# Performance work log

Hardware: AMD Instinct MI355X
Metric: run time of the kernel (lower is better)

The kernel has to match this reference:

```python
import jax, jax.numpy as jnp
import numpy as np

D = 1024
B, N = 4, 2048

def setup_inputs() -> dict:
    key = jax.random.key(0)
    ks = jax.random.split(key, 7)
    sc = 1.0 / np.sqrt(D)
    return {
        "x": jax.random.normal(ks[0], (B, N, D), dtype=jnp.float32),
        "wq_w": jax.random.normal(ks[1], (D, D), dtype=jnp.float32) * sc,
        "wq_b": jax.random.normal(ks[2], (D,), dtype=jnp.float32) * 0.01,
        "wk_w": jax.random.normal(ks[3], (D, D), dtype=jnp.float32) * sc,
        "wk_b": jax.random.normal(ks[4], (D,), dtype=jnp.float32) * 0.01,
        "wv_w": jax.random.normal(ks[5], (D, D), dtype=jnp.float32) * sc,
        "wv_b": jax.random.normal(ks[6], (D,), dtype=jnp.float32) * 0.01,
    }

def reference(x, wq_w, wq_b, wk_w, wk_b, wv_w, wv_b):
    # torch Linear: y = x @ W^T + b
    q = x @ wq_w.T + wq_b
    k = x @ wk_w.T + wk_b
    v = x @ wv_w.T + wv_b
    d = q.shape[-1]
    s = jnp.einsum("bid,bjd->bij", q, k) / jnp.sqrt(jnp.float32(d))
    # faithful to original: triu then transpose (zeros, NOT -inf, enter the softmax)
    t = jnp.swapaxes(jnp.triu(s), -2, -1)
    p = jax.nn.softmax(t, axis=-2)
    attn = jnp.swapaxes(jnp.triu(p), -2, -1) @ v
    return attn
```

## Files before the change

kernel.cpp:

```cpp
#include <hip/hip_runtime.h>
#include <hip/hip_fp16.h>
#include <cstdint>

typedef _Float16 half8_t __attribute__((ext_vector_type(8)));
typedef float f32x4 __attribute__((ext_vector_type(4)));

#define D_ 1024
#define B_ 4
#define N_ 2048
#define M_ (B_*N_)
#define NC_ 3072

#define OFF_WCAT  0u
#define OFF_BCAT  6291456u
#define OFF_XB    6303744u
#define OFF_Q     23080960u
#define OFF_K     39858176u
#define OFF_V     56635392u
#define OFF_ZP    73412608u
#define OFF_DEXP  74461184u
#define OFF_SV    74493952u

__device__ __forceinline__ void gload_lds16(const void* g, void* l) {
  __builtin_amdgcn_global_load_lds(
      (const __attribute__((address_space(1))) unsigned int*)(uintptr_t)g,
      (__attribute__((address_space(3))) unsigned int*)(uintptr_t)l, 16, 0, 0);
}

__device__ __forceinline__ void stage128x64(const __half* rowbase, char* lds, int tid) {
#pragma unroll
  for (int inst = 0; inst < 4; ++inst) {
    int L  = inst * 4096 + tid * 16;
    int r  = L >> 7;
    int cb = L & 127;
    int cbs = cb ^ ((r & 7) << 4);
    gload_lds16((const char*)rowbase + (size_t)r * (D_ * 2) + cbs, lds + L);
  }
}

__device__ __forceinline__ half8_t ldsfrag(const char* lds, int row, int cbyte) {
  int b = (row << 7) + (cbyte ^ ((row & 7) << 4));
  return *reinterpret_cast<const half8_t*>(lds + b);
}

__device__ __forceinline__ void gemm128_core(const __half* Arow0, const __half* Brow0,
                                             char* As, char* Bs, f32x4 acc[4][4]) {
  const int tid  = threadIdx.x;
  const int lane = tid & 63;
  const int wave = tid >> 6;
  const int wm = wave >> 1, wn = wave & 1;
  for (int kt = 0; kt < 16; ++kt) {
    if (kt) __syncthreads();
    stage128x64(Arow0 + kt * 64, As, tid);
    stage128x64(Brow0 + kt * 64, Bs, tid);
    asm volatile("s_waitcnt vmcnt(0)" ::: "memory");
    __syncthreads();
#pragma unroll
    for (int kk = 0; kk < 2; ++kk) {
      const int cbyte = kk * 64 + (lane >> 4) * 16;
      half8_t a[4], b[4];
#pragma unroll
      for (int mf = 0; mf < 4; ++mf) a[mf] = ldsfrag(As, wm * 64 + mf * 16 + (lane & 15), cbyte);
#pragma unroll
      for (int nf = 0; nf < 4; ++nf) b[nf] = ldsfrag(Bs, wn * 64 + nf * 16 + (lane & 15), cbyte);
#pragma unroll
      for (int mf = 0; mf < 4; ++mf)
#pragma unroll
        for (int nf = 0; nf < 4; ++nf)
          acc[mf][nf] = __builtin_amdgcn_mfma_f32_16x16x32_f16(a[mf], b[nf], acc[mf][nf], 0, 0, 0);
    }
  }
}

__device__ __forceinline__ void calc_soff(int tid, int soff[4]) {
#pragma unroll
  for (int i = 0; i < 4; ++i) {
    int L = i * 8192 + tid * 16;
    int s = L >> 10;
    int w = L & 1023;
    w ^= ((w >> 9) & 1) << 5;
    int r  = (s >> 1) * 16 + (w >> 6);
    int kb = (s & 1) * 64 + (w & 63);
    soff[i] = r * 2048 + kb;
  }
}

#define MFMA_QUAD(QM, QN)                                                     \
  _Pragma("unroll")                                                           \
  for (int ks = 0; ks < 2; ++ks)                                              \
    _Pragma("unroll")                                                         \
    for (int mf = 0; mf < 4; ++mf)                                            \
      _Pragma("unroll")                                                       \
      for (int nf = 0; nf < 2; ++nf)                                          \
        acc[(QM)*4 + mf][(QN)*2 + nf] = __builtin_amdgcn_mfma_f32_16x16x32_f16( \
            a[mf][ks], b[(QN)][nf][ks], acc[(QM)*4 + mf][(QN)*2 + nf], 0, 0, 0);

__device__ __forceinline__ void gemm256_8ph(const char* Ag, const char* Bg,
                                            char* smem, f32x4 acc[8][4]) {
  const int tid  = threadIdx.x;
  const int lane = tid & 63;
  const int wave = tid >> 6;
  const int wm = wave >> 2, wn = wave & 3;

  int soff[4];
  calc_soff(tid, soff);
  const int wlane = (((lane & 15) * 64 + (lane >> 4) * 16)) ^ (((lane >> 3) & 1) << 5);

#pragma unroll
  for (int i = 0; i < 4; ++i) gload_lds16(Ag + soff[i], smem + i * 8192 + tid * 16);
#pragma unroll
  for (int i = 0; i < 4; ++i) gload_lds16(Bg + soff[i], smem + 32768 + i * 8192 + tid * 16);
  asm volatile("s_waitcnt vmcnt(0)" ::: "memory");
  __builtin_amdgcn_s_barrier();

  for (int t = 0; t < 16; ++t) {
    char* A0  = smem + ((t & 1) << 16);
    char* B0  = A0 + 32768;
    char* A1  = smem + (((t + 1) & 1) << 16);
    char* B1s = A1 + 32768;
    const half8_t* ap = (const half8_t*)(A0 + wm * 16384 + wlane);
    const half8_t* bp = (const half8_t*)(B0 + wn * 8192 + wlane);
    const char* Agn = Ag + (t + 1) * 128;
    const char* Bgn = Bg + (t + 1) * 128;
    const bool pre = (t < 15);

    half8_t a[4][2];
    half8_t b[2][2][2];

#pragma unroll
    for (int mf = 0; mf < 4; ++mf)
#pragma unroll
      for (int ks = 0; ks < 2; ++ks)
        a[mf][ks] = ap[(mf * 2 + ks) * 64];
#pragma unroll
    for (int nf = 0; nf < 2; ++nf)
#pragma unroll
      for (int ks = 0; ks < 2; ++ks)
        b[0][nf][ks] = bp[(nf * 2 + ks) * 64];
    if (pre) {
#pragma unroll
      for (int i = 0; i < 4; ++i) gload_lds16(Agn + soff[i], A1 + i * 8192 + tid * 16);
    }
    __builtin_amdgcn_s_barrier();
    asm volatile("s_waitcnt lgkmcnt(0)" ::: "memory");
    __builtin_amdgcn_s_setprio(1);
    MFMA_QUAD(0, 0)
    __builtin_amdgcn_s_setprio(0);
    __builtin_amdgcn_s_barrier();

#pragma unroll
    for (int nf = 0; nf < 2; ++nf)
#pragma unroll
      for (int ks = 0; ks < 2; ++ks)
        b[1][nf][ks] = bp[((2 + nf) * 2 + ks) * 64];
    if (pre) {
#pragma unroll
      for (int i = 0; i < 4; ++i) gload_lds16(Bgn + soff[i], B1s + i * 8192 + tid * 16);
    }
    __builtin_amdgcn_s_barrier();
    asm volatile("s_waitcnt lgkmcnt(0)" ::: "memory");
    __builtin_amdgcn_s_setprio(1);
    MFMA_QUAD(0, 1)
    __builtin_amdgcn_s_setprio(0);
    __builtin_amdgcn_s_barrier();

#pragma unroll
    for (int mf = 0; mf < 4; ++mf)
#pragma unroll
      for (int ks = 0; ks < 2; ++ks)
        a[mf][ks] = ap[((4 + mf) * 2 + ks) * 64];
    __builtin_amdgcn_s_barrier();
    asm volatile("s_waitcnt lgkmcnt(0)" ::: "memory");
    __builtin_amdgcn_s_setprio(1);
    MFMA_QUAD(1, 0)
    __builtin_amdgcn_s_setprio(0);
    __builtin_amdgcn_s_barrier();

    __builtin_amdgcn_s_setprio(1);
    MFMA_QUAD(1, 1)
    __builtin_amdgcn_s_setprio(0);
    if (pre) asm volatile("s_waitcnt vmcnt(0)" ::: "memory");
    __builtin_amdgcn_s_barrier();
  }
}

__global__ __launch_bounds__(256) void k_prep(
    const float* __restrict__ x, const float* __restrict__ wq, const float* __restrict__ wk,
    const float* __restrict__ wv, const float* __restrict__ bq, const float* __restrict__ bk,
    const float* __restrict__ bv, __half* __restrict__ xb, __half* __restrict__ wcat,
    float* __restrict__ bcat) {
  const int NX4 = (M_ * D_) / 4;
  const int NW4 = (D_ * D_) / 4;
  const int TOT = NX4 + 3 * NW4;
  int tid0 = blockIdx.x * 256 + threadIdx.x;
  int stride = gridDim.x * 256;
  for (int i = tid0; i < TOT; i += stride) {
    float4 f; __half* dst;
    if (i < NX4) {
      f = ((const float4*)x)[i];
      dst = xb + 4 * (size_t)i;
    } else {
      int j = i - NX4; int w = j / NW4; int o = j - w * NW4;
      const float* src = (w == 0) ? wq : (w == 1) ? wk : wv;
      f = ((const float4*)src)[o];
      dst = wcat + (size_t)w * (D_ * D_) + 4 * (size_t)o;
    }
    __half h0 = __float2half(f.x), h1 = __float2half(f.y),
           h2 = __float2half(f.z), h3 = __float2half(f.w);
    ushort4 u = { __half_as_ushort(h0), __half_as_ushort(h1),
                  __half_as_ushort(h2), __half_as_ushort(h3) };
    *((ushort4*)dst) = u;
  }
  if (tid0 < NC_)
    bcat[tid0] = (tid0 < 1024) ? bq[tid0] : (tid0 < 2048) ? bk[tid0 - 1024] : bv[tid0 - 2048];
}

__global__ __launch_bounds__(256) void k_qkv(
    const __half* __restrict__ xb, const __half* __restrict__ wcat,
    const float* __restrict__ bcat,
    __half* __restrict__ q, __half* __restrict__ kx, __half* __restrict__ v,
    float* __restrict__ Sv) {
  __shared__ __align__(16) char smem[32768];
  char* As = smem; char* Bs = smem + 16384;
  int bid = blockIdx.x;
  int bm = bid / 24, bn = bid % 24;
  f32x4 acc[4][4];
#pragma unroll
  for (int i = 0; i < 4; ++i)
#pragma unroll
    for (int j = 0; j < 4; ++j) acc[i][j] = f32x4{0.f, 0.f, 0.f, 0.f};
  gemm128_core(xb + (size_t)bm * 128 * D_, wcat + (size_t)bn * 128 * D_, As, Bs, acc);

  const int lane = threadIdx.x & 63;
  const int wave = threadIdx.x >> 6;
  const int wm = wave >> 1, wn = wave & 1;
  int sel = bn >> 3;
  __half* outp = (sel == 0) ? q : (sel == 1) ? kx : v;
#pragma unroll
  for (int nf = 0; nf < 4; ++nf) {
    int nloc = wn * 64 + nf * 16 + (lane & 15);
    float bias = bcat[bn * 128 + nloc];
    int ncol = (bn & 7) * 128 + nloc;
#pragma unroll
    for (int mf = 0; mf < 4; ++mf) {
#pragma unroll
      for (int r = 0; r < 4; ++r) {
        int m = bm * 128 + wm * 64 + mf * 16 + (lane >> 4) * 4 + r;
        outp[(size_t)m * D_ + ncol] = __float2half(acc[mf][nf][r] + bias);
      }
    }
    if (sel == 2) {
      int bloc  = bm >> 4;
      int cbase = (bm & 15) * 4;
#pragma unroll
      for (int chl = 0; chl < 2; ++chl) {
        float s = 8.f * bias;
#pragma unroll
        for (int mf2 = 0; mf2 < 2; ++mf2)
#pragma unroll
          for (int r = 0; r < 4; ++r)
            s += acc[chl * 2 + mf2][nf][r];
        s += __shfl_xor(s, 16);
        s += __shfl_xor(s, 32);
        if ((lane >> 4) == 0) {
          int ch = wm * 2 + chl;
          Sv[(size_t)((bloc << 6) + cbase + ch) * D_ + ncol] = s;
        }
      }
    }
  }
}

__global__ __launch_bounds__(512, 2) void k_stats256(
    const __half* __restrict__ q, const __half* __restrict__ kx,
    float* __restrict__ Zpart, float* __restrict__ dexp) {
  __shared__ __align__(16) char smem[131072];
  int bid = blockIdx.x;
  int tile = (bid & 7) * 18 + (bid >> 3);
  int b = tile / 36;
  int r = tile % 36;
  int ti = 0;
  while (r >= 8 - ti) { r -= 8 - ti; ++ti; }
  int tj = ti + r;

  f32x4 acc[8][4];
#pragma unroll
  for (int i = 0; i < 8; ++i)
#pragma unroll
    for (int j = 0; j < 4; ++j) acc[i][j] = f32x4{0.f, 0.f, 0.f, 0.f};

  const size_t base = (size_t)b * N_ * D_;
  gemm256_8ph((const char*)(q + base + (size_t)ti * 256 * D_),
              (const char*)(kx + base + (size_t)tj * 256 * D_), smem, acc);

  const int lane = threadIdx.x & 63;
  const int wave = threadIdx.x >> 6;
  const int wm = wave >> 2, wn = wave & 3;
  const bool offd = (tj > ti);
  const float scale = 0.03125f;
  int zr0 = b * N_ + ti * 256;
#pragma unroll
  for (int mf = 0; mf < 8; ++mf) {
#pragma unroll
    for (int rr = 0; rr < 4; ++rr) {
      int il = wm * 128 + mf * 16 + (lane >> 4) * 4 + rr;
      float ssum = 0.f;
#pragma unroll
      for (int nf = 0; nf < 4; ++nf) {
        int jl = wn * 64 + nf * 16 + (lane & 15);
        float e = __expf(acc[mf][nf][rr] * scale);
        bool keep = offd || (jl >= il);
        if (!offd && jl == il) dexp[zr0 + il] = e;
        ssum += keep ? e : 0.f;
      }
      ssum += __shfl_xor(ssum, 1);
      ssum += __shfl_xor(ssum, 2);
      ssum += __shfl_xor(ssum, 4);
      ssum += __shfl_xor(ssum, 8);
      if ((lane & 15) == 0)
        Zpart[(size_t)(zr0 + il) * 32 + tj * 4 + wn] = ssum;
    }
  }
}

__global__ __launch_bounds__(256) void k_out(
    const __half* __restrict__ v, const float* __restrict__ Sv,
    const float* __restrict__ Zpart, const float* __restrict__ dexp,
    float* __restrict__ out) {
  __shared__ float sInv[32], sCd[32];
  int slab = blockIdx.x;
  int b = slab >> 6, c = slab & 63;
  int dg = threadIdx.x;
  int d0 = dg * 4;
  int zi0 = b * N_ + c * 32;

  if (dg < 32) {
    int i  = c * 32 + dg;
    int row = zi0 + dg;
    int t0 = (i >> 8) * 4;
    float z = 0.f;
    for (int t = t0; t < 32; ++t) z += Zpart[(size_t)row * 32 + t];
    float iv = 1.f / ((float)i + z);
    sInv[dg] = iv;
    sCd[dg]  = dexp[row] * iv;
  }
  __syncthreads();

  f32x4 run = {0.f, 0.f, 0.f, 0.f};
  for (int cc = 0; cc < c; ++cc) {
    f32x4 sv = *(const f32x4*)(Sv + (size_t)((b << 6) + cc) * D_ + d0);
    run[0] += sv[0]; run[1] += sv[1]; run[2] += sv[2]; run[3] += sv[3];
  }
  const ushort4* vp = (const ushort4*)(v + (size_t)zi0 * D_ + d0);
  float* op = out + (size_t)zi0 * D_ + d0;
#pragma unroll 4
  for (int r2 = 0; r2 < 32; ++r2) {
    ushort4 u = vp[r2 * (D_ / 4)];
    f32x4 vi;
    vi[0] = __half2float(__ushort_as_half(u.x));
    vi[1] = __half2float(__ushort_as_half(u.y));
    vi[2] = __half2float(__ushort_as_half(u.z));
    vi[3] = __half2float(__ushort_as_half(u.w));
    float iv = sInv[r2], cd = sCd[r2];
    f32x4 o;
    o[0] = run[0] * iv + cd * vi[0];
    o[1] = run[1] * iv + cd * vi[1];
    o[2] = run[2] * iv + cd * vi[2];
    o[3] = run[3] * iv + cd * vi[3];
    *(f32x4*)(op + (size_t)r2 * D_) = o;
    run[0] += vi[0]; run[1] += vi[1]; run[2] += vi[2]; run[3] += vi[3];
  }
}

extern "C" void kernel_launch(void* const* d_in, const int* in_sizes, int n_in,
                              void* d_out, int out_size, void* d_ws, size_t ws_size,
                              hipStream_t stream) {
  const float* x  = (const float*)d_in[0];
  const float* wq = (const float*)d_in[1];
  const float* bq = (const float*)d_in[2];
  const float* wk = (const float*)d_in[3];
  const float* bk = (const float*)d_in[4];
  const float* wv = (const float*)d_in[5];
  const float* bv = (const float*)d_in[6];
  float* out = (float*)d_out;
  char* ws = (char*)d_ws;

  __half* wcat = (__half*)(ws + OFF_WCAT);
  float*  bcat = (float*)(ws + OFF_BCAT);
  __half* xb   = (__half*)(ws + OFF_XB);
  __half* q    = (__half*)(ws + OFF_Q);
  __half* k    = (__half*)(ws + OFF_K);
  __half* v    = (__half*)(ws + OFF_V);
  float* Zpart = (float*)(ws + OFF_ZP);
  float* dexp  = (float*)(ws + OFF_DEXP);
  float* Sv    = (float*)(ws + OFF_SV);

  k_prep<<<dim3(2048), dim3(256), 0, stream>>>(x, wq, wk, wv, bq, bk, bv, xb, wcat, bcat);
  k_qkv<<<dim3(64 * 24), dim3(256), 0, stream>>>(xb, wcat, bcat, q, k, v, Sv);
  k_stats256<<<dim3(144), dim3(512), 0, stream>>>(q, k, Zpart, dexp);
  k_out<<<dim3(256), dim3(256), 0, stream>>>(v, Sv, Zpart, dexp, out);
}
```

Measured before the change: 133.7 us.

## Fold Q/K projections into a bias-augmented bilinear form x'·G·x'^T

```diff
diff --git a/kernel.cpp b/kernel.cpp
--- a/kernel.cpp
+++ b/kernel.cpp
@@ -9,17 +9,18 @@
 #define B_ 4
 #define N_ 2048
 #define M_ (B_*N_)
-#define NC_ 3072
-
-#define OFF_WCAT  0u
-#define OFF_BCAT  6291456u
-#define OFF_XB    6303744u
-#define OFF_Q     23080960u
-#define OFF_K     39858176u
-#define OFF_V     56635392u
-#define OFF_ZP    73412608u
-#define OFF_DEXP  74461184u
-#define OFF_SV    74493952u
+#define W_ 1152
+
+#define OFF_WQT   0u
+#define OFF_WKT   2097152u
+#define OFF_WV16  4194304u
+#define OFF_G2P   6291456u
+#define OFF_XB2   8945664u
+#define OFF_T2    27820032u
+#define OFF_V     46694400u
+#define OFF_ZP    63471616u
+#define OFF_DEXP  64520192u
+#define OFF_SV    64552960u
 
 __device__ __forceinline__ void gload_lds16(const void* g, void* l) {
   __builtin_amdgcn_global_load_lds(
@@ -27,14 +28,15 @@
       (__attribute__((address_space(3))) unsigned int*)(uintptr_t)l, 16, 0, 0);
 }
 
-__device__ __forceinline__ void stage128x64(const __half* rowbase, char* lds, int tid) {
+template<int LDBYTES>
+__device__ __forceinline__ void stage128x64b(const char* rowbase, char* lds, int tid) {
 #pragma unroll
   for (int inst = 0; inst < 4; ++inst) {
     int L  = inst * 4096 + tid * 16;
     int r  = L >> 7;
     int cb = L & 127;
     int cbs = cb ^ ((r & 7) << 4);
-    gload_lds16((const char*)rowbase + (size_t)r * (D_ * 2) + cbs, lds + L);
+    gload_lds16(rowbase + (size_t)r * LDBYTES + cbs, lds + L);
   }
 }
 
@@ -43,16 +45,17 @@
   return *reinterpret_cast<const half8_t*>(lds + b);
 }
 
-__device__ __forceinline__ void gemm128_core(const __half* Arow0, const __half* Brow0,
-                                             char* As, char* Bs, f32x4 acc[4][4]) {
+template<int LDA, int LDB, int NT>
+__device__ __forceinline__ void gemm128_core_t(const char* Ab, const char* Bb,
+                                               char* As, char* Bs, f32x4 acc[4][4]) {
   const int tid  = threadIdx.x;
   const int lane = tid & 63;
   const int wave = tid >> 6;
   const int wm = wave >> 1, wn = wave & 1;
-  for (int kt = 0; kt < 16; ++kt) {
+  for (int kt = 0; kt < NT; ++kt) {
     if (kt) __syncthreads();
-    stage128x64(Arow0 + kt * 64, As, tid);
-    stage128x64(Brow0 + kt * 64, Bs, tid);
+    stage128x64b<LDA>(Ab + kt * 128, As, tid);
+    stage128x64b<LDB>(Bb + kt * 128, Bs, tid);
     asm volatile("s_waitcnt vmcnt(0)" ::: "memory");
     __syncthreads();
 #pragma unroll
@@ -72,7 +75,8 @@
   }
 }
 
-__device__ __forceinline__ void calc_soff(int tid, int soff[4]) {
+template<int LDBYTES>
+__device__ __forceinline__ void calc_soff_t(int tid, int soff[4]) {
 #pragma unroll
   for (int i = 0; i < 4; ++i) {
     int L = i * 8192 + tid * 16;
@@ -81,7 +85,7 @@
     w ^= ((w >> 9) & 1) << 5;
     int r  = (s >> 1) * 16 + (w >> 6);
     int kb = (s & 1) * 64 + (w & 63);
-    soff[i] = r * 2048 + kb;
+    soff[i] = r * LDBYTES + kb;
   }
 }
 
@@ -95,25 +99,27 @@
         acc[(QM)*4 + mf][(QN)*2 + nf] = __builtin_amdgcn_mfma_f32_16x16x32_f16( \
             a[mf][ks], b[(QN)][nf][ks], acc[(QM)*4 + mf][(QN)*2 + nf], 0, 0, 0);
 
-__device__ __forceinline__ void gemm256_8ph(const char* Ag, const char* Bg,
-                                            char* smem, f32x4 acc[8][4]) {
+template<int LDA, int LDB, int NT>
+__device__ __forceinline__ void gemm256_8ph_t(const char* Ag, const char* Bg,
+                                              char* smem, f32x4 acc[8][4]) {
   const int tid  = threadIdx.x;
   const int lane = tid & 63;
   const int wave = tid >> 6;
   const int wm = wave >> 2, wn = wave & 3;
 
-  int soff[4];
-  calc_soff(tid, soff);
+  int soffA[4], soffB[4];
+  calc_soff_t<LDA>(tid, soffA);
+  calc_soff_t<LDB>(tid, soffB);
   const int wlane = (((lane & 15) * 64 + (lane >> 4) * 16)) ^ (((lane >> 3) & 1) << 5);
 
 #pragma unroll
-  for (int i = 0; i < 4; ++i) gload_lds16(Ag + soff[i], smem + i * 8192 + tid * 16);
-#pragma unroll
-  for (int i = 0; i < 4; ++i) gload_lds16(Bg + soff[i], smem + 32768 + i * 8192 + tid * 16);
+  for (int i = 0; i < 4; ++i) gload_lds16(Ag + soffA[i], smem + i * 8192 + tid * 16);
+#pragma unroll
+  for (int i = 0; i < 4; ++i) gload_lds16(Bg + soffB[i], smem + 32768 + i * 8192 + tid * 16);
   asm volatile("s_waitcnt vmcnt(0)" ::: "memory");
   __builtin_amdgcn_s_barrier();
 
-  for (int t = 0; t < 16; ++t) {
+  for (int t = 0; t < NT; ++t) {
     char* A0  = smem + ((t & 1) << 16);
     char* B0  = A0 + 32768;
     char* A1  = smem + (((t + 1) & 1) << 16);
@@ -122,7 +128,7 @@
     const half8_t* bp = (const half8_t*)(B0 + wn * 8192 + wlane);
     const char* Agn = Ag + (t + 1) * 128;
     const char* Bgn = Bg + (t + 1) * 128;
-    const bool pre = (t < 15);
+    const bool pre = (t < NT - 1);
 
     half8_t a[4][2];
     half8_t b[2][2][2];
@@ -139,7 +145,7 @@
         b[0][nf][ks] = bp[(nf * 2 + ks) * 64];
     if (pre) {
 #pragma unroll
-      for (int i = 0; i < 4; ++i) gload_lds16(Agn + soff[i], A1 + i * 8192 + tid * 16);
+      for (int i = 0; i < 4; ++i) gload_lds16(Agn + soffA[i], A1 + i * 8192 + tid * 16);
     }
     __builtin_amdgcn_s_barrier();
     asm volatile("s_waitcnt lgkmcnt(0)" ::: "memory");
@@ -155,7 +161,7 @@
         b[1][nf][ks] = bp[((2 + nf) * 2 + ks) * 64];
     if (pre) {
 #pragma unroll
-      for (int i = 0; i < 4; ++i) gload_lds16(Bgn + soff[i], B1s + i * 8192 + tid * 16);
+      for (int i = 0; i < 4; ++i) gload_lds16(Bgn + soffB[i], B1s + i * 8192 + tid * 16);
     }
     __builtin_amdgcn_s_barrier();
     asm volatile("s_waitcnt lgkmcnt(0)" ::: "memory");
@@ -187,92 +193,205 @@
 __global__ __launch_bounds__(256) void k_prep(
     const float* __restrict__ x, const float* __restrict__ wq, const float* __restrict__ wk,
     const float* __restrict__ wv, const float* __restrict__ bq, const float* __restrict__ bk,
-    const float* __restrict__ bv, __half* __restrict__ xb, __half* __restrict__ wcat,
-    float* __restrict__ bcat) {
-  const int NX4 = (M_ * D_) / 4;
-  const int NW4 = (D_ * D_) / 4;
-  const int TOT = NX4 + 3 * NW4;
-  int tid0 = blockIdx.x * 256 + threadIdx.x;
-  int stride = gridDim.x * 256;
-  for (int i = tid0; i < TOT; i += stride) {
-    float4 f; __half* dst;
-    if (i < NX4) {
-      f = ((const float4*)x)[i];
-      dst = xb + 4 * (size_t)i;
+    __half* __restrict__ xb2, __half* __restrict__ wv16,
+    __half* __restrict__ wqT, __half* __restrict__ wkT, __half* __restrict__ G2h) {
+  const int thr = threadIdx.x;
+  if (blockIdx.x < 2048) {
+    const int A_END  = 2097152;
+    const int B_END  = A_END + 262144;
+    const int C_END  = B_END + 262144;
+    const int D1_END = C_END + 36576;
+    const int D2_END = D1_END + 64512;
+    int tid0 = blockIdx.x * 256 + thr;
+    int stride = 2048 * 256;
+    for (int i = tid0; i < D2_END; i += stride) {
+      if (i < A_END) {
+        float4 f = ((const float4*)x)[i];
+        int m = i >> 8, d4 = i & 255;
+        ushort4 u = { __half_as_ushort(__float2half(f.x)), __half_as_ushort(__float2half(f.y)),
+                      __half_as_ushort(__float2half(f.z)), __half_as_ushort(__float2half(f.w)) };
+        *((ushort4*)(xb2 + (size_t)m * W_ + d4 * 4)) = u;
+      } else if (i < B_END) {
+        int j = i - A_END;
+        float4 f = ((const float4*)wv)[j];
+        ushort4 u = { __half_as_ushort(__float2half(f.x)), __half_as_ushort(__float2half(f.y)),
+                      __half_as_ushort(__float2half(f.z)), __half_as_ushort(__float2half(f.w)) };
+        *((ushort4*)(wv16 + 4 * (size_t)j)) = u;
+      } else if (i < C_END) {
+        int p = i - B_END;
+        int m = p >> 5, j4 = p & 31;
+        ushort one = 0x3C00;
+        ushort4 u = { (ushort)((j4 == 0) ? one : 0), 0, 0, 0 };
+        *((ushort4*)(xb2 + (size_t)m * W_ + 1024 + j4 * 4)) = u;
+      } else if (i < D1_END) {
+        int q = i - C_END;
+        int r = 1025 + q / 288, c4 = (q % 288) * 4;
+        ushort4 z = {0, 0, 0, 0};
+        *((ushort4*)(G2h + (size_t)r * W_ + c4)) = z;
+      } else {
+        int s = i - D1_END;
+        int r = s / 63, c = 1025 + s % 63;
+        *((ushort*)(G2h + (size_t)r * W_ + c)) = 0;
+      }
+    }
+  } else {
+    int blk = blockIdx.x - 2048;
+    if (blk < 512) {
+      const float* src = (blk < 256) ? wq : wk;
+      __half* dst = (blk < 256) ? wqT : wkT;
+      int t = blk & 255;
+      int tr = t >> 4, tc = t & 15;
+      __shared__ float tile[64][65];
+      int rr = thr >> 4;
+      int cc = (thr & 15) * 4;
+#pragma unroll
+      for (int i = 0; i < 4; ++i) {
+        int r = rr + i * 16;
+        float4 f = *(const float4*)(src + (size_t)(tr * 64 + r) * 1024 + tc * 64 + cc);
+        tile[r][cc] = f.x; tile[r][cc + 1] = f.y; tile[r][cc + 2] = f.z; tile[r][cc + 3] = f.w;
+      }
+      __syncthreads();
+#pragma unroll
+      for (int i = 0; i < 4; ++i) {
+        int r2 = rr + i * 16;
+        ushort4 u = { __half_as_ushort(__float2half(tile[cc + 0][r2])),
+                      __half_as_ushort(__float2half(tile[cc + 1][r2])),
+                      __half_as_ushort(__float2half(tile[cc + 2][r2])),
+                      __half_as_ushort(__float2half(tile[cc + 3][r2])) };
+        *((ushort4*)(dst + (size_t)(tc * 64 + r2) * 1024 + tr * 64 + cc)) = u;
+      }
+    } else if (blk < 516) {
+      int d = (blk - 512) * 256 + thr;
+      float s = 0.f;
+      for (int o = 0; o < 1024; ++o) s += wq[(size_t)o * 1024 + d] * bk[o];
+      G2h[(size_t)1024 * W_ + d] = __float2half(s);
+    } else if (blk < 520) {
+      int j = (blk - 516) * 256 + thr;
+      float s = 0.f;
+      for (int o = 0; o < 1024; ++o) s += wk[(size_t)o * 1024 + j] * bq[o];
+      G2h[(size_t)j * W_ + 1024] = __float2half(s);
     } else {
-      int j = i - NX4; int w = j / NW4; int o = j - w * NW4;
-      const float* src = (w == 0) ? wq : (w == 1) ? wk : wv;
-      f = ((const float4*)src)[o];
-      dst = wcat + (size_t)w * (D_ * D_) + 4 * (size_t)o;
-    }
-    __half h0 = __float2half(f.x), h1 = __float2half(f.y),
-           h2 = __float2half(f.z), h3 = __float2half(f.w);
-    ushort4 u = { __half_as_ushort(h0), __half_as_ushort(h1),
-                  __half_as_ushort(h2), __half_as_ushort(h3) };
-    *((ushort4*)dst) = u;
-  }
-  if (tid0 < NC_)
-    bcat[tid0] = (tid0 < 1024) ? bq[tid0] : (tid0 < 2048) ? bk[tid0 - 1024] : bv[tid0 - 2048];
-}
-
-__global__ __launch_bounds__(256) void k_qkv(
-    const __half* __restrict__ xb, const __half* __restrict__ wcat,
-    const float* __restrict__ bcat,
-    __half* __restrict__ q, __half* __restrict__ kx, __half* __restrict__ v,
-    float* __restrict__ Sv) {
+      __shared__ float red[256];
+      float s = 0.f;
+      for (int o = thr; o < 1024; o += 256) s += bq[o] * bk[o];
+      red[thr] = s;
+      __syncthreads();
+      for (int off = 128; off > 0; off >>= 1) {
+        if (thr < off) red[thr] += red[thr + off];
+        __syncthreads();
+      }
+      if (thr == 0) G2h[(size_t)1024 * W_ + 1024] = __float2half(red[0]);
+      if (thr < 127) *((ushort*)(G2h + (size_t)1024 * W_ + 1025 + thr)) = 0;
+    }
+  }
+}
+
+__global__ __launch_bounds__(256) void k_G(
+    const __half* __restrict__ wkT, const __half* __restrict__ wqT,
+    __half* __restrict__ G2h) {
   __shared__ __align__(16) char smem[32768];
-  char* As = smem; char* Bs = smem + 16384;
-  int bid = blockIdx.x;
-  int bm = bid / 24, bn = bid % 24;
+  int bm = blockIdx.x >> 3, bn = blockIdx.x & 7;
   f32x4 acc[4][4];
 #pragma unroll
   for (int i = 0; i < 4; ++i)
 #pragma unroll
     for (int j = 0; j < 4; ++j) acc[i][j] = f32x4{0.f, 0.f, 0.f, 0.f};
-  gemm128_core(xb + (size_t)bm * 128 * D_, wcat + (size_t)bn * 128 * D_, As, Bs, acc);
-
+  gemm128_core_t<2048, 2048, 16>((const char*)(wkT + (size_t)bm * 128 * 1024),
+                                 (const char*)(wqT + (size_t)bn * 128 * 1024),
+                                 smem, smem + 16384, acc);
   const int lane = threadIdx.x & 63;
   const int wave = threadIdx.x >> 6;
   const int wm = wave >> 1, wn = wave & 1;
-  int sel = bn >> 3;
-  __half* outp = (sel == 0) ? q : (sel == 1) ? kx : v;
 #pragma unroll
   for (int nf = 0; nf < 4; ++nf) {
-    int nloc = wn * 64 + nf * 16 + (lane & 15);
-    float bias = bcat[bn * 128 + nloc];
-    int ncol = (bn & 7) * 128 + nloc;
-#pragma unroll
-    for (int mf = 0; mf < 4; ++mf) {
+    int n = bn * 128 + wn * 64 + nf * 16 + (lane & 15);
+#pragma unroll
+    for (int mf = 0; mf < 4; ++mf)
 #pragma unroll
       for (int r = 0; r < 4; ++r) {
         int m = bm * 128 + wm * 64 + mf * 16 + (lane >> 4) * 4 + r;
-        outp[(size_t)m * D_ + ncol] = __float2half(acc[mf][nf][r] + bias);
-      }
-    }
-    if (sel == 2) {
-      int bloc  = bm >> 4;
-      int cbase = (bm & 15) * 4;
-#pragma unroll
-      for (int chl = 0; chl < 2; ++chl) {
-        float s = 8.f * bias;
-#pragma unroll
-        for (int mf2 = 0; mf2 < 2; ++mf2)
-#pragma unroll
-          for (int r = 0; r < 4; ++r)
-            s += acc[chl * 2 + mf2][nf][r];
-        s += __shfl_xor(s, 16);
-        s += __shfl_xor(s, 32);
-        if ((lane >> 4) == 0) {
-          int ch = wm * 2 + chl;
-          Sv[(size_t)((bloc << 6) + cbase + ch) * D_ + ncol] = s;
-        }
-      }
-    }
+        G2h[(size_t)m * W_ + n] = __float2half(acc[mf][nf][r]);
+      }
+  }
+}
+
+__global__ __launch_bounds__(256) void k_v(
+    const __half* __restrict__ xb2, const __half* __restrict__ wv16,
+    const float* __restrict__ bv, __half* __restrict__ v, float* __restrict__ Sv) {
+  __shared__ __align__(16) char smem[32768];
+  int bm = blockIdx.x >> 3, bn = blockIdx.x & 7;
+  f32x4 acc[4][4];
+#pragma unroll
+  for (int i = 0; i < 4; ++i)
+#pragma unroll
+    for (int j = 0; j < 4; ++j) acc[i][j] = f32x4{0.f, 0.f, 0.f, 0.f};
+  gemm128_core_t<2304, 2048, 16>((const char*)(xb2 + (size_t)bm * 128 * W_),
+                                 (const char*)(wv16 + (size_t)bn * 128 * 1024),
+                                 smem, smem + 16384, acc);
+  const int lane = threadIdx.x & 63;
+  const int wave = threadIdx.x >> 6;
+  const int wm = wave >> 1, wn = wave & 1;
+  int bloc = bm >> 4, cbase = (bm & 15) * 4;
+#pragma unroll
+  for (int nf = 0; nf < 4; ++nf) {
+    int ncol = bn * 128 + wn * 64 + nf * 16 + (lane & 15);
+    float bias = bv[ncol];
+#pragma unroll
+    for (int mf = 0; mf < 4; ++mf)
+#pragma unroll
+      for (int r = 0; r < 4; ++r) {
+        int m = bm * 128 + wm * 64 + mf * 16 + (lane >> 4) * 4 + r;
+        v[(size_t)m * D_ + ncol] = __float2half(acc[mf][nf][r] + bias);
+      }
+#pragma unroll
+    for (int chl = 0; chl < 2; ++chl) {
+      float s = 8.f * bias;
+#pragma unroll
+      for (int mf2 = 0; mf2 < 2; ++mf2)
+#pragma unroll
+        for (int r = 0; r < 4; ++r)
+          s += acc[chl * 2 + mf2][nf][r];
+      s += __shfl_xor(s, 16);
+      s += __shfl_xor(s, 32);
+      if ((lane >> 4) == 0) {
+        int ch = wm * 2 + chl;
+        Sv[(size_t)((bloc << 6) + cbase + ch) * D_ + ncol] = s;
+      }
+    }
+  }
+}
+
+__global__ __launch_bounds__(256) void k_t(
+    const __half* __restrict__ xb2, const __half* __restrict__ G2h,
+    __half* __restrict__ t2) {
+  __shared__ __align__(16) char smem[32768];
+  int bm = blockIdx.x / 9, bn = blockIdx.x % 9;
+  f32x4 acc[4][4];
+#pragma unroll
+  for (int i = 0; i < 4; ++i)
+#pragma unroll
+    for (int j = 0; j < 4; ++j) acc[i][j] = f32x4{0.f, 0.f, 0.f, 0.f};
+  gemm128_core_t<2304, 2304, 17>((const char*)(xb2 + (size_t)bm * 128 * W_),
+                                 (const char*)(G2h + (size_t)bn * 128 * W_),
+                                 smem, smem + 16384, acc);
+  const int lane = threadIdx.x & 63;
+  const int wave = threadIdx.x >> 6;
+  const int wm = wave >> 1, wn = wave & 1;
+#pragma unroll
+  for (int nf = 0; nf < 4; ++nf) {
+    int n = bn * 128 + wn * 64 + nf * 16 + (lane & 15);
+#pragma unroll
+    for (int mf = 0; mf < 4; ++mf)
+#pragma unroll
+      for (int r = 0; r < 4; ++r) {
+        int m = bm * 128 + wm * 64 + mf * 16 + (lane >> 4) * 4 + r;
+        t2[(size_t)m * W_ + n] = __float2half(acc[mf][nf][r]);
+      }
   }
 }
 
 __global__ __launch_bounds__(512, 2) void k_stats256(
-    const __half* __restrict__ q, const __half* __restrict__ kx,
+    const __half* __restrict__ t2, const __half* __restrict__ xb2,
     float* __restrict__ Zpart, float* __restrict__ dexp) {
   __shared__ __align__(16) char smem[131072];
   int bid = blockIdx.x;
@@ -289,9 +408,9 @@
 #pragma unroll
     for (int j = 0; j < 4; ++j) acc[i][j] = f32x4{0.f, 0.f, 0.f, 0.f};
 
-  const size_t base = (size_t)b * N_ * D_;
-  gemm256_8ph((const char*)(q + base + (size_t)ti * 256 * D_),
-              (const char*)(kx + base + (size_t)tj * 256 * D_), smem, acc);
+  gemm256_8ph_t<2304, 2304, 17>(
+      (const char*)(t2  + ((size_t)b * N_ + ti * 256) * W_),
+      (const char*)(xb2 + ((size_t)b * N_ + tj * 256) * W_), smem, acc);
 
   const int lane = threadIdx.x & 63;
   const int wave = threadIdx.x >> 6;
@@ -385,18 +504,22 @@
   float* out = (float*)d_out;
   char* ws = (char*)d_ws;
 
-  __half* wcat = (__half*)(ws + OFF_WCAT);
-  float*  bcat = (float*)(ws + OFF_BCAT);
-  __half* xb   = (__half*)(ws + OFF_XB);
-  __half* q    = (__half*)(ws + OFF_Q);
-  __half* k    = (__half*)(ws + OFF_K);
+  __half* wqT  = (__half*)(ws + OFF_WQT);
+  __half* wkT  = (__half*)(ws + OFF_WKT);
+  __half* wv16 = (__half*)(ws + OFF_WV16);
+  __half* G2h  = (__half*)(ws + OFF_G2P);
+  __half* xb2  = (__half*)(ws + OFF_XB2);
+  __half* t2   = (__half*)(ws + OFF_T2);
   __half* v    = (__half*)(ws + OFF_V);
   float* Zpart = (float*)(ws + OFF_ZP);
   float* dexp  = (float*)(ws + OFF_DEXP);
   float* Sv    = (float*)(ws + OFF_SV);
 
-  k_prep<<<dim3(2048), dim3(256), 0, stream>>>(x, wq, wk, wv, bq, bk, bv, xb, wcat, bcat);
-  k_qkv<<<dim3(64 * 24), dim3(256), 0, stream>>>(xb, wcat, bcat, q, k, v, Sv);
-  k_stats256<<<dim3(144), dim3(512), 0, stream>>>(q, k, Zpart, dexp);
+  k_prep<<<dim3(2569), dim3(256), 0, stream>>>(x, wq, wk, wv, bq, bk,
+                                               xb2, wv16, wqT, wkT, G2h);
+  k_G<<<dim3(64), dim3(256), 0, stream>>>(wkT, wqT, G2h);
+  k_v<<<dim3(512), dim3(256), 0, stream>>>(xb2, wv16, bv, v, Sv);
+  k_t<<<dim3(576), dim3(256), 0, stream>>>(xb2, G2h, t2);
+  k_stats256<<<dim3(144), dim3(512), 0, stream>>>(t2, xb2, Zpart, dexp);
   k_out<<<dim3(256), dim3(256), 0, stream>>>(v, Sv, Zpart, dexp, out);
 }
```

Measured after the change: 176.7 us. 1.32x slower.

## Split QKV projection; overlap V projection with QK stats via atomic work queue

Applied to the files above, without the earlier changes.

```diff
diff --git a/kernel.cpp b/kernel.cpp
--- a/kernel.cpp
+++ b/kernel.cpp
@@ -20,56 +20,12 @@
 #define OFF_ZP    73412608u
 #define OFF_DEXP  74461184u
 #define OFF_SV    74493952u
+#define OFF_QC    75542528u
 
 __device__ __forceinline__ void gload_lds16(const void* g, void* l) {
   __builtin_amdgcn_global_load_lds(
       (const __attribute__((address_space(1))) unsigned int*)(uintptr_t)g,
       (__attribute__((address_space(3))) unsigned int*)(uintptr_t)l, 16, 0, 0);
-}
-
-__device__ __forceinline__ void stage128x64(const __half* rowbase, char* lds, int tid) {
-#pragma unroll
-  for (int inst = 0; inst < 4; ++inst) {
-    int L  = inst * 4096 + tid * 16;
-    int r  = L >> 7;
-    int cb = L & 127;
-    int cbs = cb ^ ((r & 7) << 4);
-    gload_lds16((const char*)rowbase + (size_t)r * (D_ * 2) + cbs, lds + L);
-  }
-}
-
-__device__ __forceinline__ half8_t ldsfrag(const char* lds, int row, int cbyte) {
-  int b = (row << 7) + (cbyte ^ ((row & 7) << 4));
-  return *reinterpret_cast<const half8_t*>(lds + b);
-}
-
-__device__ __forceinline__ void gemm128_core(const __half* Arow0, const __half* Brow0,
-                                             char* As, char* Bs, f32x4 acc[4][4]) {
-  const int tid  = threadIdx.x;
-  const int lane = tid & 63;
-  const int wave = tid >> 6;
-  const int wm = wave >> 1, wn = wave & 1;
-  for (int kt = 0; kt < 16; ++kt) {
-    if (kt) __syncthreads();
-    stage128x64(Arow0 + kt * 64, As, tid);
-    stage128x64(Brow0 + kt * 64, Bs, tid);
-    asm volatile("s_waitcnt vmcnt(0)" ::: "memory");
-    __syncthreads();
-#pragma unroll
-    for (int kk = 0; kk < 2; ++kk) {
-      const int cbyte = kk * 64 + (lane >> 4) * 16;
-      half8_t a[4], b[4];
-#pragma unroll
-      for (int mf = 0; mf < 4; ++mf) a[mf] = ldsfrag(As, wm * 64 + mf * 16 + (lane & 15), cbyte);
-#pragma unroll
-      for (int nf = 0; nf < 4; ++nf) b[nf] = ldsfrag(Bs, wn * 64 + nf * 16 + (lane & 15), cbyte);
-#pragma unroll
-      for (int mf = 0; mf < 4; ++mf)
-#pragma unroll
-        for (int nf = 0; nf < 4; ++nf)
-          acc[mf][nf] = __builtin_amdgcn_mfma_f32_16x16x32_f16(a[mf], b[nf], acc[mf][nf], 0, 0, 0);
-    }
-  }
 }
 
 __device__ __forceinline__ void calc_soff(int tid, int soff[4]) {
@@ -215,73 +171,14 @@
     bcat[tid0] = (tid0 < 1024) ? bq[tid0] : (tid0 < 2048) ? bk[tid0 - 1024] : bv[tid0 - 2048];
 }
 
-__global__ __launch_bounds__(256) void k_qkv(
+__global__ __launch_bounds__(512, 2) void k_qk(
     const __half* __restrict__ xb, const __half* __restrict__ wcat,
     const float* __restrict__ bcat,
-    __half* __restrict__ q, __half* __restrict__ kx, __half* __restrict__ v,
-    float* __restrict__ Sv) {
-  __shared__ __align__(16) char smem[32768];
-  char* As = smem; char* Bs = smem + 16384;
-  int bid = blockIdx.x;
-  int bm = bid / 24, bn = bid % 24;
-  f32x4 acc[4][4];
-#pragma unroll
-  for (int i = 0; i < 4; ++i)
-#pragma unroll
-    for (int j = 0; j < 4; ++j) acc[i][j] = f32x4{0.f, 0.f, 0.f, 0.f};
-  gemm128_core(xb + (size_t)bm * 128 * D_, wcat + (size_t)bn * 128 * D_, As, Bs, acc);
-
-  const int lane = threadIdx.x & 63;
-  const int wave = threadIdx.x >> 6;
-  const int wm = wave >> 1, wn = wave & 1;
-  int sel = bn >> 3;
-  __half* outp = (sel == 0) ? q : (sel == 1) ? kx : v;
-#pragma unroll
-  for (int nf = 0; nf < 4; ++nf) {
-    int nloc = wn * 64 + nf * 16 + (lane & 15);
-    float bias = bcat[bn * 128 + nloc];
-    int ncol = (bn & 7) * 128 + nloc;
-#pragma unroll
-    for (int mf = 0; mf < 4; ++mf) {
-#pragma unroll
-      for (int r = 0; r < 4; ++r) {
-        int m = bm * 128 + wm * 64 + mf * 16 + (lane >> 4) * 4 + r;
-        outp[(size_t)m * D_ + ncol] = __float2half(acc[mf][nf][r] + bias);
-      }
-    }
-    if (sel == 2) {
-      int bloc  = bm >> 4;
-      int cbase = (bm & 15) * 4;
-#pragma unroll
-      for (int chl = 0; chl < 2; ++chl) {
-        float s = 8.f * bias;
-#pragma unroll
-        for (int mf2 = 0; mf2 < 2; ++mf2)
-#pragma unroll
-          for (int r = 0; r < 4; ++r)
-            s += acc[chl * 2 + mf2][nf][r];
-        s += __shfl_xor(s, 16);
-        s += __shfl_xor(s, 32);
-        if ((lane >> 4) == 0) {
-          int ch = wm * 2 + chl;
-          Sv[(size_t)((bloc << 6) + cbase + ch) * D_ + ncol] = s;
-        }
-      }
-    }
-  }
-}
-
-__global__ __launch_bounds__(512, 2) void k_stats256(
-    const __half* __restrict__ q, const __half* __restrict__ kx,
-    float* __restrict__ Zpart, float* __restrict__ dexp) {
+    __half* __restrict__ q, __half* __restrict__ kx) {
   __shared__ __align__(16) char smem[131072];
   int bid = blockIdx.x;
-  int tile = (bid & 7) * 18 + (bid >> 3);
-  int b = tile / 36;
-  int r = tile % 36;
-  int ti = 0;
-  while (r >= 8 - ti) { r -= 8 - ti; ++ti; }
-  int tj = ti + r;
+  int tile = (bid & 7) * 32 + (bid >> 3);
+  int bm = tile >> 3, bn = tile & 7;
 
   f32x4 acc[8][4];
 #pragma unroll
@@ -289,36 +186,131 @@
 #pragma unroll
     for (int j = 0; j < 4; ++j) acc[i][j] = f32x4{0.f, 0.f, 0.f, 0.f};
 
-  const size_t base = (size_t)b * N_ * D_;
-  gemm256_8ph((const char*)(q + base + (size_t)ti * 256 * D_),
-              (const char*)(kx + base + (size_t)tj * 256 * D_), smem, acc);
+  gemm256_8ph((const char*)(xb + (size_t)bm * 256 * D_),
+              (const char*)(wcat + (size_t)bn * 256 * D_), smem, acc);
 
   const int lane = threadIdx.x & 63;
   const int wave = threadIdx.x >> 6;
   const int wm = wave >> 2, wn = wave & 3;
-  const bool offd = (tj > ti);
-  const float scale = 0.03125f;
-  int zr0 = b * N_ + ti * 256;
-#pragma unroll
-  for (int mf = 0; mf < 8; ++mf) {
-#pragma unroll
-    for (int rr = 0; rr < 4; ++rr) {
-      int il = wm * 128 + mf * 16 + (lane >> 4) * 4 + rr;
-      float ssum = 0.f;
-#pragma unroll
-      for (int nf = 0; nf < 4; ++nf) {
-        int jl = wn * 64 + nf * 16 + (lane & 15);
-        float e = __expf(acc[mf][nf][rr] * scale);
-        bool keep = offd || (jl >= il);
-        if (!offd && jl == il) dexp[zr0 + il] = e;
-        ssum += keep ? e : 0.f;
+  __half* outp = (bn < 4) ? q : kx;
+  int colbase = (bn & 3) * 256 + wn * 64;
+#pragma unroll
+  for (int nf = 0; nf < 4; ++nf) {
+    int col = colbase + nf * 16 + (lane & 15);
+    float bias = bcat[bn * 256 + wn * 64 + nf * 16 + (lane & 15)];
+#pragma unroll
+    for (int mf = 0; mf < 8; ++mf) {
+#pragma unroll
+      for (int rr = 0; rr < 4; ++rr) {
+        int m = bm * 256 + wm * 128 + mf * 16 + (lane >> 4) * 4 + rr;
+        outp[(size_t)m * D_ + col] = __float2half(acc[mf][nf][rr] + bias);
       }
-      ssum += __shfl_xor(ssum, 1);
-      ssum += __shfl_xor(ssum, 2);
-      ssum += __shfl_xor(ssum, 4);
-      ssum += __shfl_xor(ssum, 8);
-      if ((lane & 15) == 0)
-        Zpart[(size_t)(zr0 + il) * 32 + tj * 4 + wn] = ssum;
+    }
+  }
+}
+
+__global__ __launch_bounds__(512, 2) void k_statsv(
+    const __half* __restrict__ q, const __half* __restrict__ kx,
+    const __half* __restrict__ xb, const __half* __restrict__ wcat,
+    const float* __restrict__ bcat,
+    __half* __restrict__ v, float* __restrict__ Sv,
+    float* __restrict__ Zpart, float* __restrict__ dexp, int* __restrict__ qc) {
+  __shared__ __align__(16) char smem[131072];
+  __shared__ int s_vt;
+  const int thr  = threadIdx.x;
+  const int lane = thr & 63;
+  const int wave = thr >> 6;
+  const int wm = wave >> 2, wn = wave & 3;
+
+  int bid = blockIdx.x;
+  int tile = (bid & 7) * 32 + (bid >> 3);
+
+  if (tile < 144) {
+    int b = tile / 36;
+    int r = tile % 36;
+    int ti = 0;
+    while (r >= 8 - ti) { r -= 8 - ti; ++ti; }
+    int tj = ti + r;
+
+    f32x4 acc[8][4];
+#pragma unroll
+    for (int i = 0; i < 8; ++i)
+#pragma unroll
+      for (int j = 0; j < 4; ++j) acc[i][j] = f32x4{0.f, 0.f, 0.f, 0.f};
+
+    const size_t base = (size_t)b * N_ * D_;
+    gemm256_8ph((const char*)(q + base + (size_t)ti * 256 * D_),
+                (const char*)(kx + base + (size_t)tj * 256 * D_), smem, acc);
+
+    const bool offd = (tj > ti);
+    const float scale = 0.03125f;
+    int zr0 = b * N_ + ti * 256;
+#pragma unroll
+    for (int mf = 0; mf < 8; ++mf) {
+#pragma unroll
+      for (int rr = 0; rr < 4; ++rr) {
+        int il = wm * 128 + mf * 16 + (lane >> 4) * 4 + rr;
+        float ssum = 0.f;
+#pragma unroll
+        for (int nf = 0; nf < 4; ++nf) {
+          int jl = wn * 64 + nf * 16 + (lane & 15);
+          float e = __expf(acc[mf][nf][rr] * scale);
+          bool keep = offd || (jl >= il);
+          if (!offd && jl == il) dexp[zr0 + il] = e;
+          ssum += keep ? e : 0.f;
+        }
+        ssum += __shfl_xor(ssum, 1);
+        ssum += __shfl_xor(ssum, 2);
+        ssum += __shfl_xor(ssum, 4);
+        ssum += __shfl_xor(ssum, 8);
+        if ((lane & 15) == 0)
+          Zpart[(size_t)(zr0 + il) * 32 + tj * 4 + wn] = ssum;
+      }
+    }
+  }
+
+  for (;;) {
+    __syncthreads();
+    if (thr == 0) s_vt = atomicAdd(qc, 1);
+    __syncthreads();
+    int vt = s_vt;
+    if (vt >= 128) break;
+    int bm = vt >> 2, bn = vt & 3;
+
+    f32x4 acc[8][4];
+#pragma unroll
+    for (int i = 0; i < 8; ++i)
+#pragma unroll
+      for (int j = 0; j < 4; ++j) acc[i][j] = f32x4{0.f, 0.f, 0.f, 0.f};
+
+    gemm256_8ph((const char*)(xb + (size_t)bm * 256 * D_),
+                (const char*)(wcat + (size_t)(2048 + bn * 256) * D_), smem, acc);
+
+#pragma unroll
+    for (int nf = 0; nf < 4; ++nf) {
+      int col = bn * 256 + wn * 64 + nf * 16 + (lane & 15);
+      float bias = bcat[2048 + col];
+#pragma unroll
+      for (int mf = 0; mf < 8; ++mf) {
+#pragma unroll
+        for (int rr = 0; rr < 4; ++rr) {
+          int m = bm * 256 + wm * 128 + mf * 16 + (lane >> 4) * 4 + rr;
+          v[(size_t)m * D_ + col] = __float2half(acc[mf][nf][rr] + bias);
+        }
+      }
+#pragma unroll
+      for (int t = 0; t < 4; ++t) {
+        float s = 8.f * bias;
+#pragma unroll
+        for (int dd = 0; dd < 2; ++dd)
+#pragma unroll
+          for (int rr = 0; rr < 4; ++rr)
+            s += acc[t * 2 + dd][nf][rr];
+        s += __shfl_xor(s, 16);
+        s += __shfl_xor(s, 32);
+        if ((lane >> 4) == 0)
+          Sv[(size_t)(bm * 8 + wm * 4 + t) * D_ + col] = s;
+      }
     }
   }
 }
@@ -394,9 +386,11 @@
   float* Zpart = (float*)(ws + OFF_ZP);
   float* dexp  = (float*)(ws + OFF_DEXP);
   float* Sv    = (float*)(ws + OFF_SV);
-
+  int*   qc    = (int*)(ws + OFF_QC);
+
+  hipMemsetAsync((void*)qc, 0, 256, stream);
   k_prep<<<dim3(2048), dim3(256), 0, stream>>>(x, wq, wk, wv, bq, bk, bv, xb, wcat, bcat);
-  k_qkv<<<dim3(64 * 24), dim3(256), 0, stream>>>(xb, wcat, bcat, q, k, v, Sv);
-  k_stats256<<<dim3(144), dim3(512), 0, stream>>>(q, k, Zpart, dexp);
+  k_qk<<<dim3(256), dim3(512), 0, stream>>>(xb, wcat, bcat, q, k);
+  k_statsv<<<dim3(256), dim3(512), 0, stream>>>(q, k, xb, wcat, bcat, v, Sv, Zpart, dexp, qc);
   k_out<<<dim3(256), dim3(256), 0, stream>>>(v, Sv, Zpart, dexp, out);
 }
```

New measurement: 145.7 us. 1.09x slower.
